# Performance work log

Hardware: AMD Instinct MI355X
Metric: run time of the kernel (lower is better)

The kernel has to match this reference:

```python
import jax, jax.numpy as jnp
import numpy as np

B, N, C, H = 8, 4096, 1024, 16
D = C // H            # head_dim = 64
SCALE = D ** -0.5


def setup_inputs() -> dict:
    key = jax.random.key(0)
    k1, k2, k3 = jax.random.split(key, 3)
    x = jax.random.normal(k1, (B, N, C), dtype=jnp.float32)
    w_qkv = jax.random.normal(k2, (C, 3 * C), dtype=jnp.float32) * 0.02
    w_proj = jax.random.normal(k3, (C, C), dtype=jnp.float32) * 0.02
    b_proj = jnp.zeros((C,), dtype=jnp.float32)
    return {"x": x, "w_qkv": w_qkv, "w_proj": w_proj, "b_proj": b_proj}


def reference(x, w_qkv, w_proj, b_proj):
    # Faithful translation of the TF module, INCLUDING its missing head-permute:
    # after unstack, q/k/v are (B, N, H, D); tf.matmul batches over (B, N),
    # so attention is an (H x H) softmax over heads, per token.
    Bv, Nv, Cv = x.shape
    qkv = (x @ w_qkv).reshape(Bv, Nv, 3, H, D)          # qkv has no bias (qkv_bias=False)
    q, k, v = qkv[:, :, 0], qkv[:, :, 1], qkv[:, :, 2]   # each (B, N, H, D)
    q = q * SCALE
    attn = jnp.einsum("bnhd,bngd->bnhg", q, k)           # (B, N, H, H)
    attn = jax.nn.softmax(attn, axis=-1)
    o = jnp.einsum("bnhg,bngd->bnhd", attn, v)           # (B, N, H, D)
    o = jnp.transpose(o, (0, 2, 1, 3)).reshape(Bv, Nv, Cv)  # literal transpose+reshape
    return o @ w_proj + b_proj
```

## Files before the change

### kernel.cpp

```cpp
#include <hip/hip_runtime.h>
#include <hip/hip_bf16.h>
#include <stdint.h>

typedef __attribute__((ext_vector_type(8))) short short8;
typedef __attribute__((ext_vector_type(4))) float f32x4;
typedef unsigned short ushort_t;

#define VMCNT4 asm volatile("s_waitcnt vmcnt(4)" ::: "memory")
#define VMCNT0 asm volatile("s_waitcnt vmcnt(0)" ::: "memory")
#define LGKM0  asm volatile("s_waitcnt lgkmcnt(0)" ::: "memory")
#define BARRIER asm volatile("s_barrier" ::: "memory")

__device__ inline ushort_t f2bf(float f) {
    union { float f; unsigned u; } v; v.f = f;
    unsigned u = v.u;
    unsigned r = u + 0x7fffu + ((u >> 16) & 1u);
    return (ushort_t)(r >> 16);
}

__device__ inline void gload_lds16(const void* g, void* l) {
    __builtin_amdgcn_global_load_lds((const __attribute__((address_space(1))) void*)g,
                                     (__attribute__((address_space(3))) void*)l,
                                     16, 0, 0);
}

__device__ inline short8 read_frag(const ushort_t* region, int r, int c) {
    int byte = (r << 7) + (c << 1);
    byte ^= (r & 7) << 4;
    return *(const short8*)((const char*)region + byte);
}

#define MFMA16(AF, MB, NB, BF)                                                    \
    _Pragma("unroll")                                                             \
    for (int mi = 0; mi < 4; ++mi)                                                \
        _Pragma("unroll")                                                         \
        for (int ni = 0; ni < 2; ++ni)                                            \
            _Pragma("unroll")                                                     \
            for (int ks = 0; ks < 2; ++ks)                                        \
                acc[(MB) + mi][(NB) + ni] = __builtin_amdgcn_mfma_f32_16x16x32_bf16( \
                    AF[mi * 2 + ks], BF[ni * 2 + ks], acc[(MB) + mi][(NB) + ni], 0, 0, 0);

template <int F32OUT>
__global__ __launch_bounds__(512, 2) void gemm256(const ushort_t* __restrict__ A,
                                                  const ushort_t* __restrict__ Bt,
                                                  void* __restrict__ Cc,
                                                  const float* __restrict__ bias,
                                                  int N, int K, int NBN, int LT) {
    __shared__ __align__(16) ushort_t lds[65536];
    const int tid = threadIdx.x;
    const int wave = tid >> 6;
    const int lane = tid & 63;
    const int wm = wave >> 2;
    const int wn = wave & 3;
    const int el = (lane & 56) | ((lane ^ (lane >> 3)) & 7);
    const int NT = K >> 6;
    const int NTM = NT - 1;

    auto tile_of = [&](int lt, int& obm, int& obn) {
        int x = (lt & 7) * (LT >> 3) + (lt >> 3);
        int per = NBN << 3;
        int st = x / per;
        int rem = x - st * per;
        obn = rem >> 3;
        obm = (st << 3) + (rem & 7);
    };

    auto STAGE = [&](const ushort_t* g, int rowHalf, int k0, int regionByteOff) {
#pragma unroll
        for (int j = 0; j < 2; ++j) {
            int e = j * 4096 + wave * 512 + el * 8;
            gload_lds16(g + (size_t)(rowHalf + (e >> 6)) * K + k0 + (e & 63),
                        (char*)lds + regionByteOff + j * 8192 + wave * 1024);
        }
    };

    int bm, bn;
    tile_of((int)blockIdx.x, bm, bn);
    const ushort_t* Ag = A + (size_t)bm * 256 * K;
    const ushort_t* Bg = Bt + (size_t)bn * 256 * K;

    STAGE(Ag, 0,   0, 0);
    STAGE(Ag, 128, 0, 16384);
    STAGE(Bg, 0,   0, 65536);
    STAGE(Bg, 128, 0, 65536 + 16384);
    STAGE(Bg, 0,   64, 65536 + 32768);
    STAGE(Bg, 128, 64, 65536 + 49152);
    VMCNT4;
    BARRIER;

    f32x4 acc[8][4] = {};
    short8 aF[8], aG[8], bF0[4], bF1[4];
    const f32x4 zf = {0.f, 0.f, 0.f, 0.f};
    const int ra = lane & 15;
    const int ca = (lane >> 4) << 3;
    const int rb = (wn & 1) << 6;

    for (int lt = (int)blockIdx.x; lt < LT; lt += 256) {
        const bool hasN = (lt + 256) < LT;
        int bmN = bm, bnN = bn;
        const ushort_t* AgN = Ag;
        const ushort_t* BgN = Bg;
        if (hasN) {
            tile_of(lt + 256, bmN, bnN);
            AgN = A + (size_t)bmN * 256 * K;
            BgN = Bt + (size_t)bnN * 256 * K;
        }

        for (int it = 0; it < NT; ++it) {
            const int s = it & 1;
            const ushort_t* Ar = lds + ((s << 1) + wm) * 8192;
            const ushort_t* Br = lds + 32768 + ((s << 1) + (wn >> 1)) * 8192;
            const int itA = it + 1, itB = it + 2;
            const bool doA = (itA < NT) || hasN;
            const bool doB = (itB < NT) || hasN;
            const ushort_t* As = (itA < NT) ? Ag : AgN;
            const ushort_t* Bs = (itB < NT) ? Bg : BgN;
            const int kA = (itA & NTM) << 6;
            const int kB = (itB & NTM) << 6;
            const int soA = ((s ^ 1) << 1) * 16384;
            const int soB = 65536 + (s << 1) * 16384;

#pragma unroll
            for (int mi = 0; mi < 4; ++mi)
#pragma unroll
                for (int ks = 0; ks < 2; ++ks)
                    aF[mi * 2 + ks] = read_frag(Ar, mi * 16 + ra, ks * 32 + ca);
#pragma unroll
            for (int ni = 0; ni < 2; ++ni)
#pragma unroll
                for (int ks = 0; ks < 2; ++ks)
                    bF0[ni * 2 + ks] = read_frag(Br, rb + ni * 16 + ra, ks * 32 + ca);
            if (doA) STAGE(As, 0, kA, soA);
            BARRIER; LGKM0;
            __builtin_amdgcn_s_setprio(1);
            MFMA16(aF, 0, 0, bF0)
            __builtin_amdgcn_s_setprio(0);

#pragma unroll
            for (int ni = 0; ni < 2; ++ni)
#pragma unroll
                for (int ks = 0; ks < 2; ++ks)
                    bF1[ni * 2 + ks] = read_frag(Br, rb + 32 + ni * 16 + ra, ks * 32 + ca);
            if (doA) STAGE(As, 128, kA, soA + 16384);
            BARRIER; LGKM0;
            __builtin_amdgcn_s_setprio(1);
            MFMA16(aF, 0, 2, bF1)
            __builtin_amdgcn_s_setprio(0);

#pragma unroll
            for (int mi = 0; mi < 4; ++mi)
#pragma unroll
                for (int ks = 0; ks < 2; ++ks)
                    aG[mi * 2 + ks] = read_frag(Ar, 64 + mi * 16 + ra, ks * 32 + ca);
            BARRIER; LGKM0;
            if (doB) STAGE(Bs, 0, kB, soB);
            __builtin_amdgcn_s_setprio(1);
            MFMA16(aG, 4, 0, bF0)
            __builtin_amdgcn_s_setprio(0);

            if (doB) STAGE(Bs, 128, kB, soB + 16384);
            __builtin_amdgcn_s_setprio(1);
            MFMA16(aG, 4, 2, bF1)
            __builtin_amdgcn_s_setprio(0);
            if (doB) { VMCNT4; } else { VMCNT0; }
            BARRIER;
        }

        const int row0 = bm * 256 + wm * 128 + (lane >> 4) * 4;
        const int col0 = bn * 256 + wn * 64 + (lane & 15);
#pragma unroll
        for (int mi = 0; mi < 8; ++mi) {
#pragma unroll
            for (int ni = 0; ni < 4; ++ni) {
                const int col = col0 + ni * 16;
                f32x4 v = acc[mi][ni];
                if constexpr (F32OUT) {
                    float bz = bias[col];
                    float* C = (float*)Cc;
#pragma unroll
                    for (int q = 0; q < 4; ++q)
                        C[(size_t)(row0 + mi * 16 + q) * N + col] = v[q] + bz;
                } else {
                    ushort_t* C = (ushort_t*)Cc;
#pragma unroll
                    for (int q = 0; q < 4; ++q)
                        C[(size_t)(row0 + mi * 16 + q) * N + col] = f2bf(v[q]);
                }
                acc[mi][ni] = zf;
            }
        }
        Ag = AgN; Bg = BgN; bm = bmN; bn = bnN;
    }
}

__global__ __launch_bounds__(256) void prep_kernel(const float* __restrict__ x,
                                                   ushort_t* __restrict__ x_bf,
                                                   const float* __restrict__ w_qkv,
                                                   ushort_t* __restrict__ wq_t,
                                                   const float* __restrict__ w_proj,
                                                   ushort_t* __restrict__ wp_t) {
    const int blk = blockIdx.x;
    const int t = threadIdx.x;
    if (blk < 2048) {
        const int n8 = 33554432 / 8;
        int i = blk * 256 + t;
        const int stride = 2048 * 256;
        for (; i < n8; i += stride) {
            const float4* p = (const float4*)(x + (size_t)i * 8);
            float4 a = p[0];
            float4 b = p[1];
            uint4 w;
            w.x = (unsigned)f2bf(a.x) | ((unsigned)f2bf(a.y) << 16);
            w.y = (unsigned)f2bf(a.z) | ((unsigned)f2bf(a.w) << 16);
            w.z = (unsigned)f2bf(b.x) | ((unsigned)f2bf(b.y) << 16);
            w.w = (unsigned)f2bf(b.z) | ((unsigned)f2bf(b.w) << 16);
            *(uint4*)(x_bf + (size_t)i * 8) = w;
        }
        return;
    }
    const float* in;
    ushort_t* out;
    int Cn, c0, r0;
    if (blk < 2048 + 768) {
        int id = blk - 2048;
        in = w_qkv; out = wq_t; Cn = 3072;
        c0 = (id % 48) * 64; r0 = (id / 48) * 64;
    } else {
        int id = blk - 2048 - 768;
        in = w_proj; out = wp_t; Cn = 1024;
        c0 = (id % 16) * 64; r0 = (id / 16) * 64;
    }
    __shared__ float tile[64][65];
    int lr = t >> 4;
    int lc = (t & 15) * 4;
#pragma unroll
    for (int i = 0; i < 4; i++) {
        const float* src = in + (size_t)(r0 + i * 16 + lr) * Cn + c0 + lc;
        float4 v = *(const float4*)src;
        tile[i * 16 + lr][lc + 0] = v.x;
        tile[i * 16 + lr][lc + 1] = v.y;
        tile[i * 16 + lr][lc + 2] = v.z;
        tile[i * 16 + lr][lc + 3] = v.w;
    }
    __syncthreads();
    int oc = t >> 4;
    int ok = (t & 15) * 4;
#pragma unroll
    for (int i = 0; i < 4; i++) {
        int c = c0 + i * 16 + oc;
        ushort4 w;
        w.x = f2bf(tile[ok + 0][i * 16 + oc]);
        w.y = f2bf(tile[ok + 1][i * 16 + oc]);
        w.z = f2bf(tile[ok + 2][i * 16 + oc]);
        w.w = f2bf(tile[ok + 3][i * 16 + oc]);
        *(ushort4*)(out + (size_t)c * 1024 + r0 + ok) = w;
    }
}

__global__ __launch_bounds__(256) void attn_kernel(const ushort_t* __restrict__ qkv,
                                                   ushort_t* __restrict__ operm) {
    __shared__ __align__(16) float plds[4][16 * 20];
    const int wave = threadIdx.x >> 6;
    const int lane = threadIdx.x & 63;
    float* P = plds[wave];
    const int fr = lane & 15;
    const int fo = (lane >> 4) * 8;
    int tok = (blockIdx.x * 4 + wave) * 4;
    for (int it = 0; it < 4; it++, tok++) {
        const ushort_t* row = qkv + (size_t)tok * 3072;
        short8 aq0 = *(const short8*)(row + fr * 64 + fo);
        short8 aq1 = *(const short8*)(row + fr * 64 + 32 + fo);
        short8 bk0 = *(const short8*)(row + 1024 + fr * 64 + fo);
        short8 bk1 = *(const short8*)(row + 1024 + fr * 64 + 32 + fo);
        f32x4 s = {0.f, 0.f, 0.f, 0.f};
        s = __builtin_amdgcn_mfma_f32_16x16x32_bf16(aq0, bk0, s, 0, 0, 0);
        s = __builtin_amdgcn_mfma_f32_16x16x32_bf16(aq1, bk1, s, 0, 0, 0);
        float ls[4], m[4], p[4], sm[4];
#pragma unroll
        for (int q = 0; q < 4; q++) { ls[q] = s[q] * 0.125f; m[q] = ls[q]; }
#pragma unroll
        for (int d = 1; d < 16; d <<= 1)
#pragma unroll
            for (int q = 0; q < 4; q++) m[q] = fmaxf(m[q], __shfl_xor(m[q], d));
#pragma unroll
        for (int q = 0; q < 4; q++) { p[q] = __expf(ls[q] - m[q]); sm[q] = p[q]; }
#pragma unroll
        for (int d = 1; d < 16; d <<= 1)
#pragma unroll
            for (int q = 0; q < 4; q++) sm[q] += __shfl_xor(sm[q], d);
#pragma unroll
        for (int q = 0; q < 4; q++) P[((lane >> 4) * 4 + q) * 20 + fr] = p[q];
        __syncthreads();
        short8 pa = {};
        if (lane < 32) {
            const float* src = P + fr * 20 + fo;
            float4 r0 = *(const float4*)src;
            float4 r1 = *(const float4*)(src + 4);
            pa[0] = (short)f2bf(r0.x); pa[1] = (short)f2bf(r0.y);
            pa[2] = (short)f2bf(r0.z); pa[3] = (short)f2bf(r0.w);
            pa[4] = (short)f2bf(r1.x); pa[5] = (short)f2bf(r1.y);
            pa[6] = (short)f2bf(r1.z); pa[7] = (short)f2bf(r1.w);
        }
        __syncthreads();
        f32x4 o[4] = {};
        const ushort_t* vrow = row + 2048;
#pragma unroll
        for (int db = 0; db < 4; db++) {
            short8 bv = {};
            if (lane < 32) {
#pragma unroll
                for (int j = 0; j < 8; j++)
                    bv[j] = (short)vrow[(fo + j) * 64 + db * 16 + fr];
            }
            o[db] = __builtin_amdgcn_mfma_f32_16x16x32_bf16(pa, bv, o[db], 0, 0, 0);
        }
        float inv[4];
#pragma unroll
        for (int q = 0; q < 4; q++) inv[q] = 1.0f / sm[q];
        int b = tok >> 12;
        int n = tok & 4095;
        ushort_t* obase = operm + ((size_t)b << 22);
        int rlo = n >> 4;
        int cbase = (n & 15) * 64;
#pragma unroll
        for (int db = 0; db < 4; db++) {
#pragma unroll
            for (int q = 0; q < 4; q++) {
                int h = (lane >> 4) * 4 + q;
                int d = db * 16 + fr;
                obase[(size_t)(h * 256 + rlo) * 1024 + cbase + d] = f2bf(o[db][q] * inv[q]);
            }
        }
    }
}

extern "C" void kernel_launch(void* const* d_in, const int* in_sizes, int n_in,
                              void* d_out, int out_size, void* d_ws, size_t ws_size,
                              hipStream_t stream) {
    const float* x = (const float*)d_in[0];
    const float* w_qkv = (const float*)d_in[1];
    const float* w_proj = (const float*)d_in[2];
    const float* b_proj = (const float*)d_in[3];
    float* out = (float*)d_out;

    char* ws = (char*)d_ws;
    ushort_t* x_bf  = (ushort_t*)(ws);
    ushort_t* wq_t  = (ushort_t*)(ws + 67108864);
    ushort_t* wp_t  = (ushort_t*)(ws + 73400320);
    ushort_t* qkv   = (ushort_t*)(ws + 75497472);
    ushort_t* operm = (ushort_t*)(ws + 276824064);

    prep_kernel<<<3072, 256, 0, stream>>>(x, x_bf, w_qkv, wq_t, w_proj, wp_t);
    gemm256<0><<<256, 512, 0, stream>>>(x_bf, wq_t, qkv, nullptr, 3072, 1024, 12, 1536);
    attn_kernel<<<2048, 256, 0, stream>>>(qkv, operm);
    gemm256<1><<<256, 512, 0, stream>>>(operm, wp_t, out, b_proj, 1024, 1024, 4, 512);
}
```

Before: 394.2 us.

## Stage V transpose and output tile through LDS, drop block barriers in attention

```diff
diff --git a/kernel.cpp b/kernel.cpp
--- a/kernel.cpp
+++ b/kernel.cpp
@@ -259,12 +259,21 @@
 
 __global__ __launch_bounds__(256) void attn_kernel(const ushort_t* __restrict__ qkv,
                                                    ushort_t* __restrict__ operm) {
-    __shared__ __align__(16) float plds[4][16 * 20];
+    __shared__ __align__(16) ushort_t vtl[4][1024];
+    __shared__ __align__(16) float pl[4][16 * 20];
+    __shared__ __align__(16) ushort_t oll[4][16 * 72];
     const int wave = threadIdx.x >> 6;
     const int lane = threadIdx.x & 63;
-    float* P = plds[wave];
+    ushort_t* VT = vtl[wave];
+    float* P = pl[wave];
+    ushort_t* OL = oll[wave];
     const int fr = lane & 15;
-    const int fo = (lane >> 4) * 8;
+    const int hs = lane >> 4;
+    const int fo = hs * 8;
+    const int vg = lane & 15;
+    const int vdq = lane >> 4;
+    const int oh = lane >> 2;
+    const int od = (lane & 3) * 16;
     int tok = (blockIdx.x * 4 + wave) * 4;
     for (int it = 0; it < 4; it++, tok++) {
         const ushort_t* row = qkv + (size_t)tok * 3072;
@@ -272,9 +281,23 @@
         short8 aq1 = *(const short8*)(row + fr * 64 + 32 + fo);
         short8 bk0 = *(const short8*)(row + 1024 + fr * 64 + fo);
         short8 bk1 = *(const short8*)(row + 1024 + fr * 64 + 32 + fo);
+        short8 v0 = *(const short8*)(row + 2048 + vg * 64 + vdq * 16);
+        short8 v1 = *(const short8*)(row + 2048 + vg * 64 + vdq * 16 + 8);
         f32x4 s = {0.f, 0.f, 0.f, 0.f};
         s = __builtin_amdgcn_mfma_f32_16x16x32_bf16(aq0, bk0, s, 0, 0, 0);
         s = __builtin_amdgcn_mfma_f32_16x16x32_bf16(aq1, bk1, s, 0, 0, 0);
+#pragma unroll
+        for (int j = 0; j < 8; ++j) {
+            int d = vdq * 16 + j;
+            int slot = (2 * d + (vg >> 3)) ^ (2 * vdq);
+            VT[slot * 8 + (vg & 7)] = (ushort_t)v0[j];
+        }
+#pragma unroll
+        for (int j = 0; j < 8; ++j) {
+            int d = vdq * 16 + 8 + j;
+            int slot = (2 * d + (vg >> 3)) ^ (2 * vdq);
+            VT[slot * 8 + (vg & 7)] = (ushort_t)v1[j];
+        }
         float ls[4], m[4], p[4], sm[4];
 #pragma unroll
         for (int q = 0; q < 4; q++) { ls[q] = s[q] * 0.125f; m[q] = ls[q]; }
@@ -289,9 +312,10 @@
 #pragma unroll
             for (int q = 0; q < 4; q++) sm[q] += __shfl_xor(sm[q], d);
 #pragma unroll
-        for (int q = 0; q < 4; q++) P[((lane >> 4) * 4 + q) * 20 + fr] = p[q];
-        __syncthreads();
+        for (int q = 0; q < 4; q++) P[(hs * 4 + q) * 20 + fr] = p[q];
+        LGKM0;
         short8 pa = {};
+        short8 bv[4] = {};
         if (lane < 32) {
             const float* src = P + fr * 20 + fo;
             float4 r0 = *(const float4*)src;
@@ -300,37 +324,35 @@
             pa[2] = (short)f2bf(r0.z); pa[3] = (short)f2bf(r0.w);
             pa[4] = (short)f2bf(r1.x); pa[5] = (short)f2bf(r1.y);
             pa[6] = (short)f2bf(r1.z); pa[7] = (short)f2bf(r1.w);
-        }
-        __syncthreads();
+#pragma unroll
+            for (int db = 0; db < 4; ++db) {
+                int d = db * 16 + fr;
+                int slot = (2 * d + hs) ^ (2 * db);
+                bv[db] = *(const short8*)(VT + slot * 8);
+            }
+        }
         f32x4 o[4] = {};
-        const ushort_t* vrow = row + 2048;
-#pragma unroll
-        for (int db = 0; db < 4; db++) {
-            short8 bv = {};
-            if (lane < 32) {
-#pragma unroll
-                for (int j = 0; j < 8; j++)
-                    bv[j] = (short)vrow[(fo + j) * 64 + db * 16 + fr];
-            }
-            o[db] = __builtin_amdgcn_mfma_f32_16x16x32_bf16(pa, bv, o[db], 0, 0, 0);
-        }
+#pragma unroll
+        for (int db = 0; db < 4; db++)
+            o[db] = __builtin_amdgcn_mfma_f32_16x16x32_bf16(pa, bv[db], o[db], 0, 0, 0);
         float inv[4];
 #pragma unroll
         for (int q = 0; q < 4; q++) inv[q] = 1.0f / sm[q];
+#pragma unroll
+        for (int db = 0; db < 4; db++)
+#pragma unroll
+            for (int q = 0; q < 4; q++)
+                OL[(hs * 4 + q) * 72 + db * 16 + fr] = f2bf(o[db][q] * inv[q]);
+        LGKM0;
         int b = tok >> 12;
         int n = tok & 4095;
-        ushort_t* obase = operm + ((size_t)b << 22);
-        int rlo = n >> 4;
-        int cbase = (n & 15) * 64;
-#pragma unroll
-        for (int db = 0; db < 4; db++) {
-#pragma unroll
-            for (int q = 0; q < 4; q++) {
-                int h = (lane >> 4) * 4 + q;
-                int d = db * 16 + fr;
-                obase[(size_t)(h * 256 + rlo) * 1024 + cbase + d] = f2bf(o[db][q] * inv[q]);
-            }
-        }
+        short8 w0 = *(const short8*)(OL + oh * 72 + od);
+        short8 w1 = *(const short8*)(OL + oh * 72 + od + 8);
+        ushort_t* dst = operm + ((size_t)b << 22)
+                      + ((size_t)(oh * 256 + (n >> 4))) * 1024 + (n & 15) * 64 + od;
+        *(short8*)dst = w0;
+        *(short8*)(dst + 8) = w1;
+        LGKM0;
     }
 }
 
```

After: 375.9 us. 1.05x faster.
